# Kernel tuning notes

Hardware: AMD Instinct MI355X
Metric: run time of the kernel (lower is better)

## Reference

```python
import jax, jax.numpy as jnp
import numpy as np

N = 8192
EARTH_R = 6371.0      # km
MAX_DIST = 300.0      # max_distance_km
THRESHOLD = 0.3


def setup_inputs() -> dict:
    key = jax.random.key(0)
    k1, k2, k3, k4 = jax.random.split(key, 4)
    lat = 25.0 + 25.0 * jax.random.uniform(k1, (N,), dtype=jnp.float32)    # 25..50 N
    lon = -125.0 + 60.0 * jax.random.uniform(k2, (N,), dtype=jnp.float32)  # -125..-65 E
    positions = jnp.stack([lat, lon], axis=1)                              # [N, 2]
    wind_speed = 15.0 * jax.random.uniform(k3, (N,), dtype=jnp.float32)    # 0..15 m/s
    wind_direction = 360.0 * jax.random.uniform(k4, (N,), dtype=jnp.float32)
    return {"positions": positions, "wind_speed": wind_speed, "wind_direction": wind_direction}


def reference(positions, wind_speed, wind_direction):
    # Dense, vectorized equivalent of the original O(N^2) scalar loop.
    # Returns the dense influence matrix (edge weights, zero where no edge)
    # and the boolean edge mask; edge_index = nonzero(mask) off-device.
    lat = jnp.radians(positions[:, 0])
    lon = jnp.radians(positions[:, 1])
    lat1, lat2 = lat[:, None], lat[None, :]          # i = source row, j = target col
    dlat = lat2 - lat1                                # [N, N]
    dlon = lon[None, :] - lon[:, None]

    # Haversine distance (km)
    a = jnp.sin(dlat / 2) ** 2 + jnp.cos(lat1) * jnp.cos(lat2) * jnp.sin(dlon / 2) ** 2
    a = jnp.clip(a, 1e-12, 1.0 - 1e-12)  # avoid sqrt(0)/sqrt(<0) issues on diagonal
    dist = 2.0 * EARTH_R * jnp.arctan2(jnp.sqrt(a), jnp.sqrt(1.0 - a))

    # Bearing from i to j (degrees in [0, 360))
    x = jnp.sin(dlon) * jnp.cos(lat2)
    y = jnp.cos(lat1) * jnp.sin(lat2) - jnp.sin(lat1) * jnp.cos(lat2) * jnp.cos(dlon)
    eye = jnp.eye(positions.shape[0], dtype=bool)
    x = jnp.where(eye, 0.0, x)  # guard atan2(0,0) on diagonal (masked out anyway)
    y = jnp.where(eye, 1.0, y)
    bearing = (jnp.degrees(jnp.arctan2(x, y)) + 360.0) % 360.0

    # Wind/bearing alignment and influence score
    angle_diff = jnp.abs((bearing - wind_direction[:, None] + 180.0) % 360.0 - 180.0)
    alignment = jnp.cos(jnp.radians(angle_diff))
    influence = alignment * (wind_speed[:, None] / 10.0) * jnp.exp(-dist / 100.0)

    mask = (~eye) & (dist <= MAX_DIST) & (influence > THRESHOLD)
    edge_attr_dense = jnp.where(mask, influence, 0.0)  # [N, N]
    return edge_attr_dense, mask
```

## Files before the change

### kernel.cpp

```cpp
#include <hip/hip_runtime.h>
#include <math.h>


#define NN 8192
#define TI 32
#define TJ 4096

#define ACUT 1.9e-4f

typedef float floatx4 __attribute__((ext_vector_type(4)));

__global__ __launch_bounds__(1024) void dyn_graph_kernel(
    const float* __restrict__ pos,
    const float* __restrict__ wspd,
    const float* __restrict__ wdir,
    float* __restrict__ out)
{
    __shared__ __align__(16) float irow[TI * 12];

    const int tid   = threadIdx.x;
    const int i0    = blockIdx.y * TI;
    const int jbase = blockIdx.x * TJ + tid * 4;

    const float DEG2RAD = 0.017453292519943295f;

    if (tid < TI) {
        int i = i0 + tid;
        float latr = pos[2 * i]     * DEG2RAD;
        float lonr = pos[2 * i + 1] * DEG2RAD;
        float wr   = wdir[i]        * DEG2RAD;
        float s, c, hs, hc, hsl, hcl, sl, cl, swr, cwr;
        sincosf(latr,        &s,   &c);
        sincosf(0.5f * latr, &hs,  &hc);
        sincosf(0.5f * lonr, &hsl, &hcl);
        sincosf(lonr,        &sl,  &cl);
        sincosf(wr,          &swr, &cwr);
        float* p = &irow[tid * 12];
        p[0] = s;   p[1] = c;   p[2]  = hs;  p[3]  = hc;
        p[4] = hsl; p[5] = hcl; p[6]  = sl;  p[7]  = cl;
        p[8] = swr; p[9] = cwr; p[10] = wspd[i] / 10.0f;
        p[11] = 0.0f;
    }

    float4 p01 = *(const float4*)(pos + 2 * jbase);
    float4 p23 = *(const float4*)(pos + 2 * jbase + 4);
    float jlat[4] = { p01.x, p01.z, p23.x, p23.z };
    float jlon[4] = { p01.y, p01.w, p23.y, p23.w };

    float js[4], jc[4], jhs[4], jhc[4], jhsl[4], jhcl[4], jsl[4], jcl[4];
    #pragma unroll
    for (int k = 0; k < 4; ++k) {
        float latr = jlat[k] * DEG2RAD;
        float lonr = jlon[k] * DEG2RAD;
        sincosf(latr,        &js[k],   &jc[k]);
        sincosf(0.5f * latr, &jhs[k],  &jhc[k]);
        sincosf(0.5f * lonr, &jhsl[k], &jhcl[k]);
        sincosf(lonr,        &jsl[k],  &jcl[k]);
    }

    __syncthreads();

    unsigned long long mlo = 0ULL, mhi = 0ULL;

    #pragma unroll 2
    for (int r = 0; r < TI; ++r) {
        const float4* p4 = (const float4*)&irow[r * 12];
        float4 A = p4[0], B = p4[1], C = p4[2];
        const float is  = A.x, ic  = A.y, ihs = A.z, ihc = A.w;
        const float ihsl= B.x, ihcl= B.y, isl = B.z, icl = B.w;
        const float swr = C.x, cwr = C.y, ws10= C.z;
        const int i = i0 + r;

        float ev[4];
        unsigned int nib = 0u;
        #pragma unroll
        for (int k = 0; k < 4; ++k) {
            float shlat = jhs[k] * ihc - jhc[k] * ihs;
            float shlon = jhsl[k] * ihcl - jhcl[k] * ihsl;
            float cc = ic * jc[k];
            float a = shlat * shlat + cc * (shlon * shlon);

            ev[k] = 0.0f;

            if (a <= ACUT) {
                float ac = fmaxf(a, 1e-12f);
                float sq = sqrtf(ac);
                float dist = 12742.0f * sq * __builtin_fmaf(ac, 0.16666667f, 1.0f);

                float sdlon = jsl[k] * icl - jcl[k] * isl;
                float cdlon = jcl[k] * icl + jsl[k] * isl;
                float x = sdlon * jc[k];
                float y = ic * js[k] - (is * jc[k]) * cdlon;

                float num = y * cwr + x * swr;
                float h2  = x * x + y * y;
                float align = num * rsqrtf(h2);

                float infl = align * ws10 * __expf(dist * -0.01f);
                bool m = (jbase + k != i) && (infl > 0.3f);
                ev[k] = m ? infl : 0.0f;
                nib |= (m ? 1u : 0u) << k;
            }
        }

        unsigned long long val = (unsigned long long)nib << ((4 * r) & 63);
        mlo |= (r < 16) ? val : 0ULL;
        mhi |= (r < 16) ? 0ULL : val;

        size_t idx = (size_t)i * NN + jbase;
        floatx4 evv = { ev[0], ev[1], ev[2], ev[3] };
        __builtin_nontemporal_store(evv, (floatx4*)(out + idx));
    }

    float* outm = out + (size_t)NN * NN;
    #pragma unroll
    for (int r = 0; r < TI; ++r) {
        unsigned int nib = (unsigned int)(((r < 16 ? mlo : mhi) >> (4 * (r & 15))) & 0xFULL);
        floatx4 mvv = { (float)(nib & 1u), (float)((nib >> 1) & 1u),
                        (float)((nib >> 2) & 1u), (float)((nib >> 3) & 1u) };
        size_t idx = (size_t)(i0 + r) * NN + jbase;
        __builtin_nontemporal_store(mvv, (floatx4*)(outm + idx));
    }
}

extern "C" void kernel_launch(void* const* d_in, const int* in_sizes, int n_in,
                              void* d_out, int out_size, void* d_ws, size_t ws_size,
                              hipStream_t stream) {
    const float* pos  = (const float*)d_in[0];
    const float* wspd = (const float*)d_in[1];
    const float* wdir = (const float*)d_in[2];
    float* out = (float*)d_out;

    dim3 grid(NN / TJ, NN / TI);
    dim3 block(1024);
    dyn_graph_kernel<<<grid, block, 0, stream>>>(pos, wspd, wdir, out);
}
```

Before: 529.1 us.

## Widen tile to full row with eight columns per thread and fewer rows

Each thread now handles eight target columns instead of four, a block covers the whole row of 8192 columns, and the row tile shrinks from 32 to 16. The per-column trig setup is amortized over more work per thread and issued by fewer blocks overall, and the stores become pairs of 16-byte writes. The cost is higher register pressure from the doubled per-column arrays, and each block now processes fewer rows against that setup.

```diff
diff --git a/kernel.cpp b/kernel.cpp
--- a/kernel.cpp
+++ b/kernel.cpp
@@ -3,8 +3,8 @@
 
 
 #define NN 8192
-#define TI 32
-#define TJ 4096
+#define TI 16
+#define TJ 8192
 
 #define ACUT 1.9e-4f
 
@@ -20,7 +20,7 @@
 
     const int tid   = threadIdx.x;
     const int i0    = blockIdx.y * TI;
-    const int jbase = blockIdx.x * TJ + tid * 4;
+    const int jbase = tid * 8;
 
     const float DEG2RAD = 0.017453292519943295f;
 
@@ -42,14 +42,16 @@
         p[11] = 0.0f;
     }
 
-    float4 p01 = *(const float4*)(pos + 2 * jbase);
-    float4 p23 = *(const float4*)(pos + 2 * jbase + 4);
-    float jlat[4] = { p01.x, p01.z, p23.x, p23.z };
-    float jlon[4] = { p01.y, p01.w, p23.y, p23.w };
+    float4 q0 = *(const float4*)(pos + 2 * jbase);
+    float4 q1 = *(const float4*)(pos + 2 * jbase + 4);
+    float4 q2 = *(const float4*)(pos + 2 * jbase + 8);
+    float4 q3 = *(const float4*)(pos + 2 * jbase + 12);
+    float jlat[8] = { q0.x, q0.z, q1.x, q1.z, q2.x, q2.z, q3.x, q3.z };
+    float jlon[8] = { q0.y, q0.w, q1.y, q1.w, q2.y, q2.w, q3.y, q3.w };
 
-    float js[4], jc[4], jhs[4], jhc[4], jhsl[4], jhcl[4], jsl[4], jcl[4];
+    float js[8], jc[8], jhs[8], jhc[8], jhsl[8], jhcl[8], jsl[8], jcl[8];
     #pragma unroll
-    for (int k = 0; k < 4; ++k) {
+    for (int k = 0; k < 8; ++k) {
         float latr = jlat[k] * DEG2RAD;
         float lonr = jlon[k] * DEG2RAD;
         sincosf(latr,        &js[k],   &jc[k]);
@@ -71,10 +73,10 @@
         const float swr = C.x, cwr = C.y, ws10= C.z;
         const int i = i0 + r;
 
-        float ev[4];
-        unsigned int nib = 0u;
+        float ev[8];
+        unsigned int byte = 0u;
         #pragma unroll
-        for (int k = 0; k < 4; ++k) {
+        for (int k = 0; k < 8; ++k) {
             float shlat = jhs[k] * ihc - jhc[k] * ihs;
             float shlon = jhsl[k] * ihcl - jhcl[k] * ihsl;
             float cc = ic * jc[k];
@@ -99,27 +101,32 @@
                 float infl = align * ws10 * __expf(dist * -0.01f);
                 bool m = (jbase + k != i) && (infl > 0.3f);
                 ev[k] = m ? infl : 0.0f;
-                nib |= (m ? 1u : 0u) << k;
+                byte |= (m ? 1u : 0u) << k;
             }
         }
 
-        unsigned long long val = (unsigned long long)nib << ((4 * r) & 63);
-        mlo |= (r < 16) ? val : 0ULL;
-        mhi |= (r < 16) ? 0ULL : val;
+        unsigned long long val = (unsigned long long)byte << ((8 * r) & 63);
+        mlo |= (r < 8) ? val : 0ULL;
+        mhi |= (r < 8) ? 0ULL : val;
 
         size_t idx = (size_t)i * NN + jbase;
-        floatx4 evv = { ev[0], ev[1], ev[2], ev[3] };
-        __builtin_nontemporal_store(evv, (floatx4*)(out + idx));
+        floatx4 e0 = { ev[0], ev[1], ev[2], ev[3] };
+        floatx4 e1 = { ev[4], ev[5], ev[6], ev[7] };
+        __builtin_nontemporal_store(e0, (floatx4*)(out + idx));
+        __builtin_nontemporal_store(e1, (floatx4*)(out + idx + 4));
     }
 
     float* outm = out + (size_t)NN * NN;
     #pragma unroll
     for (int r = 0; r < TI; ++r) {
-        unsigned int nib = (unsigned int)(((r < 16 ? mlo : mhi) >> (4 * (r & 15))) & 0xFULL);
-        floatx4 mvv = { (float)(nib & 1u), (float)((nib >> 1) & 1u),
-                        (float)((nib >> 2) & 1u), (float)((nib >> 3) & 1u) };
+        unsigned int byte = (unsigned int)(((r < 8 ? mlo : mhi) >> (8 * (r & 7))) & 0xFFULL);
+        floatx4 m0 = { (float)(byte & 1u),        (float)((byte >> 1) & 1u),
+                       (float)((byte >> 2) & 1u), (float)((byte >> 3) & 1u) };
+        floatx4 m1 = { (float)((byte >> 4) & 1u), (float)((byte >> 5) & 1u),
+                       (float)((byte >> 6) & 1u), (float)((byte >> 7) & 1u) };
         size_t idx = (size_t)(i0 + r) * NN + jbase;
-        __builtin_nontemporal_store(mvv, (floatx4*)(outm + idx));
+        __builtin_nontemporal_store(m0, (floatx4*)(outm + idx));
+        __builtin_nontemporal_store(m1, (floatx4*)(outm + idx + 4));
     }
 }
 
@@ -131,7 +138,7 @@
     const float* wdir = (const float*)d_in[2];
     float* out = (float*)d_out;
 
-    dim3 grid(NN / TJ, NN / TI);
+    dim3 grid(1, NN / TI);
     dim3 block(1024);
     dyn_graph_kernel<<<grid, block, 0, stream>>>(pos, wspd, wdir, out);
 }
```

Measured after the change: 680.8 us. 28.7% more time.
